# Kernel tuning notes

Hardware: AMD Instinct MI355X
Metric: run time of the kernel (lower is better)

The kernel has to match this reference:

```python
import jax, jax.numpy as jnp
import numpy as np

B = 4        # batch_size
S = 128      # input spatial grid size per dim (shape=[128,128,128])
C = 64       # feature channels
N = 500000   # active voxels
K = 2        # kernel_size == stride (non-overlapping sparse max pool)


def setup_inputs() -> dict:
    key = jax.random.key(0)
    kf, kb, ks = jax.random.split(key, 3)
    features = jax.random.normal(kf, (N, C), dtype=jnp.float32)
    b = jax.random.randint(kb, (N, 1), 0, B, dtype=jnp.int32)
    zyx = jax.random.randint(ks, (N, 3), 0, S, dtype=jnp.int32)
    coors = jnp.concatenate([b, zyx], axis=1)  # [N, 4] = (batch, z, y, x)
    return {"features": features, "coors": coors}


def reference(features, coors):
    # Layer 1: sparse 2x2x2/stride-2 max pool == segment-max over output voxel ids.
    S1 = S // K  # 64
    b = coors[:, 0]
    z = coors[:, 1] // K
    y = coors[:, 2] // K
    x = coors[:, 3] // K
    seg = ((b * S1 + z) * S1 + y) * S1 + x  # flat output-site id
    nseg = B * S1 * S1 * S1
    # scatter-max: empty segments become -inf (inactive sites)
    dense = jax.ops.segment_max(features, seg, num_segments=nseg)
    cnt = jax.ops.segment_sum(jnp.ones((N,), jnp.int32), seg, num_segments=nseg)
    mask1 = (cnt > 0).reshape(B, S1, S1, S1)
    dense = dense.reshape(B, S1, S1, S1, C)

    # Layer 2: same pooling on the (now grid-aligned) active sites.
    # -inf at inactive sites makes block-max equal to max over active sites only.
    S2 = S1 // K  # 32
    blocks = dense.reshape(B, S2, K, S2, K, S2, K, C)
    pooled = blocks.max(axis=(2, 4, 6))               # [B, S2, S2, S2, C]
    mask2 = mask1.reshape(B, S2, K, S2, K, S2, K).any(axis=(2, 4, 6))
    out = jnp.where(mask2[..., None], pooled, jnp.float32(0.0))
    return out
```

## Files before the change

kernel.cpp:

```cpp
#include <hip/hip_runtime.h>

#define NB 4
#define S_OUT 32
#define NC 64
#define OUT_CELLS (NB * S_OUT * S_OUT * S_OUT)
#define OUT_ELEMS (OUT_CELLS * NC)
#define NGROUPS (OUT_CELLS / 4)
#define CAP 16
#define OVF_CAP 65536

typedef float floatx4 __attribute__((ext_vector_type(4)));


__global__ void fill_kernel(const int4* __restrict__ coors,
                            int* __restrict__ cnt,
                            int* __restrict__ list,
                            int* __restrict__ ovf_cnt,
                            int* __restrict__ ovf,
                            int n_pts) {
    int p = blockIdx.x * blockDim.x + threadIdx.x;
    if (p >= n_pts) return;
    int4 co = coors[p];
    int cell = ((co.x * S_OUT + (co.y >> 2)) * S_OUT + (co.z >> 2)) * S_OUT + (co.w >> 2);
    int slot = atomicAdd(&cnt[cell], 1);
    if (slot < CAP) {
        list[cell * CAP + slot] = p;
    } else {
        int o = atomicAdd(ovf_cnt, 1);
        if (o < OVF_CAP) ovf[o] = p;
    }
}

__global__ __launch_bounds__(256) void gather_kernel(
        const float* __restrict__ features,
        const int4* __restrict__ coors,
        const int* __restrict__ cnt,
        const int* __restrict__ list,
        const int* __restrict__ ovf_cnt,
        const int* __restrict__ ovf,
        float* __restrict__ out) {
    const int lane  = threadIdx.x & 63;
    const int wid   = (blockIdx.x * blockDim.x + threadIdx.x) >> 6;
    const int nw    = (gridDim.x * blockDim.x) >> 6;
    const int cl    = (lane & 15) << 2;
    const int sbase = lane & 48;
    const int qsel  = lane >> 4;

    int g = wid;
    if (g >= NGROUPS) return;

    int n_pf  = cnt[(g << 2) + qsel];
    int pl_pf = list[((size_t)g << 6) + lane];

    while (true) {
        int n  = n_pf;
        int pl = pl_pf;
        int gn = g + nw;
        if (gn < NGROUPS) {
            n_pf  = cnt[(gn << 2) + qsel];
            pl_pf = list[((size_t)gn << 6) + lane];
        }

        int m = n < CAP ? n : CAP;
        float4 acc = make_float4(-INFINITY, -INFINITY, -INFINITY, -INFINITY);

        #pragma unroll
        for (int s = 0; s < 8; ++s) {
            int p = __shfl(pl, sbase + s);
            bool v = s < m;
            int ps = v ? p : 0;
            const float4 f = *(const float4*)(features + (size_t)ps * NC + cl);
            if (v) {
                acc.x = fmaxf(acc.x, f.x); acc.y = fmaxf(acc.y, f.y);
                acc.z = fmaxf(acc.z, f.z); acc.w = fmaxf(acc.w, f.w);
            }
        }
        if (m > 8) {
            for (int s = 8; s < m; ++s) {
                int p = __shfl(pl, sbase + s);
                const float4 f = *(const float4*)(features + (size_t)p * NC + cl);
                acc.x = fmaxf(acc.x, f.x); acc.y = fmaxf(acc.y, f.y);
                acc.z = fmaxf(acc.z, f.z); acc.w = fmaxf(acc.w, f.w);
            }
        }
        if (__builtin_expect(__any(n > CAP), 0)) {
            int mycell = (g << 2) + qsel;
            int novf = *ovf_cnt;
            if (novf > OVF_CAP) novf = OVF_CAP;
            for (int i = 0; i < novf; ++i) {
                int p = ovf[i];
                int4 co = coors[p];
                int cellp = ((co.x * S_OUT + (co.y >> 2)) * S_OUT + (co.z >> 2)) * S_OUT + (co.w >> 2);
                if (n > CAP && cellp == mycell) {
                    const float4 f = *(const float4*)(features + (size_t)p * NC + cl);
                    acc.x = fmaxf(acc.x, f.x); acc.y = fmaxf(acc.y, f.y);
                    acc.z = fmaxf(acc.z, f.z); acc.w = fmaxf(acc.w, f.w);
                }
            }
        }
        if (n == 0) acc = make_float4(0.f, 0.f, 0.f, 0.f);
        floatx4 accv = { acc.x, acc.y, acc.z, acc.w };
        __builtin_nontemporal_store(accv, (floatx4*)(out + ((size_t)g << 8) + (size_t)lane * 4));

        if (gn >= NGROUPS) break;
        g = gn;
    }
}


__device__ __forceinline__ unsigned flip_f(float f) {
    unsigned u = __float_as_uint(f);
    return (u & 0x80000000u) ? ~u : (u | 0x80000000u);
}
__device__ __forceinline__ float unflip_f(unsigned u) {
    unsigned v = (u & 0x80000000u) ? (u & 0x7FFFFFFFu) : ~u;
    return __uint_as_float(v);
}

__global__ void init_kernel(uint4* __restrict__ out4, int n4) {
    int i = blockIdx.x * blockDim.x + threadIdx.x;
    int stride = gridDim.x * blockDim.x;
    uint4 z = make_uint4(0u, 0u, 0u, 0u);
    for (; i < n4; i += stride) out4[i] = z;
}

__global__ void scatter_kernel(const float* __restrict__ features,
                               const int4* __restrict__ coors,
                               unsigned* __restrict__ acc, int n_pts) {
    int gid = blockIdx.x * blockDim.x + threadIdx.x;
    int p = gid >> 6;
    int c = threadIdx.x & 63;
    if (p >= n_pts) return;
    int4 co = coors[p];
    int cell = ((co.x * S_OUT + (co.y >> 2)) * S_OUT + (co.z >> 2)) * S_OUT + (co.w >> 2);
    atomicMax(acc + (size_t)cell * NC + c, flip_f(features[(size_t)p * NC + c]));
}

__global__ void finalize_kernel(unsigned* __restrict__ acc, int n) {
    int i = blockIdx.x * blockDim.x + threadIdx.x;
    int stride = gridDim.x * blockDim.x;
    for (; i < n; i += stride) {
        unsigned u = acc[i];
        ((float*)acc)[i] = (u == 0u) ? 0.0f : unflip_f(u);
    }
}

extern "C" void kernel_launch(void* const* d_in, const int* in_sizes, int n_in,
                              void* d_out, int out_size, void* d_ws, size_t ws_size,
                              hipStream_t stream) {
    const float* features = (const float*)d_in[0];
    const int4*  coors    = (const int4*)d_in[1];
    int n_pts = in_sizes[0] / NC;

    const size_t off_cnt  = 0;
    const size_t cnt_b    = (size_t)OUT_CELLS * 4;
    const size_t off_ovfc = cnt_b;
    const size_t off_ovf  = off_ovfc + 256;
    const size_t off_list = off_ovf + (size_t)OVF_CAP * 4;
    const size_t need     = off_list + (size_t)OUT_CELLS * CAP * 4;

    if (ws_size >= need) {
        char* ws = (char*)d_ws;
        int* cnt     = (int*)(ws + off_cnt);
        int* ovf_cnt = (int*)(ws + off_ovfc);
        int* ovf     = (int*)(ws + off_ovf);
        int* list    = (int*)(ws + off_list);
        float* out   = (float*)d_out;

        (void)hipMemsetAsync(ws, 0, off_ovfc + 4, stream);

        {
            int block = 256;
            int grid = (n_pts + block - 1) / block;
            fill_kernel<<<grid, block, 0, stream>>>(coors, cnt, list, ovf_cnt, ovf, n_pts);
        }
        {
            int block = 256;
            int grid = 2048;
            gather_kernel<<<grid, block, 0, stream>>>(features, coors, cnt, list,
                                                      ovf_cnt, ovf, out);
        }
    } else {
        unsigned* acc = (unsigned*)d_out;
        init_kernel<<<2048, 256, 0, stream>>>((uint4*)d_out, OUT_ELEMS / 4);
        int grid = (n_pts * 64 + 255) / 256;
        scatter_kernel<<<grid, 256, 0, stream>>>(features, coors, acc, n_pts);
        finalize_kernel<<<2048, 256, 0, stream>>>(acc, OUT_ELEMS);
    }
}
```

Before: 63.95 us.

## Software-pipeline gather kernel with double-buffered feature loads across four groups

Replaces the grid-stride loop in the gather kernel with a fully unrolled, fixed four-groups-per-wave schedule. Loads for the first eight points of the next group are issued into a second register set while the current group is reduced, so more memory requests stay in flight per wave. This assumes NGROUPS equals exactly four times the wave count, which holds for the hard-coded grid but drops the bounds check and raises register pressure, which may reduce occupancy.

```diff
diff --git a/kernel.cpp b/kernel.cpp
--- a/kernel.cpp
+++ b/kernel.cpp
@@ -8,6 +8,8 @@
 #define NGROUPS (OUT_CELLS / 4)
 #define CAP 16
 #define OVF_CAP 65536
+#define GATHER_BLOCKS 2048
+#define NWAVES (GATHER_BLOCKS * 4)
 
 typedef float floatx4 __attribute__((ext_vector_type(4)));
 
@@ -41,70 +43,88 @@
         float* __restrict__ out) {
     const int lane  = threadIdx.x & 63;
     const int wid   = (blockIdx.x * blockDim.x + threadIdx.x) >> 6;
-    const int nw    = (gridDim.x * blockDim.x) >> 6;
     const int cl    = (lane & 15) << 2;
     const int sbase = lane & 48;
     const int qsel  = lane >> 4;
 
-    int g = wid;
-    if (g >= NGROUPS) return;
-
-    int n_pf  = cnt[(g << 2) + qsel];
-    int pl_pf = list[((size_t)g << 6) + lane];
-
-    while (true) {
-        int n  = n_pf;
-        int pl = pl_pf;
-        int gn = g + nw;
-        if (gn < NGROUPS) {
-            n_pf  = cnt[(gn << 2) + qsel];
-            pl_pf = list[((size_t)gn << 6) + lane];
-        }
-
-        int m = n < CAP ? n : CAP;
-        float4 acc = make_float4(-INFINITY, -INFINITY, -INFINITY, -INFINITY);
-
-        #pragma unroll
-        for (int s = 0; s < 8; ++s) {
-            int p = __shfl(pl, sbase + s);
-            bool v = s < m;
-            int ps = v ? p : 0;
-            const float4 f = *(const float4*)(features + (size_t)ps * NC + cl);
-            if (v) {
-                acc.x = fmaxf(acc.x, f.x); acc.y = fmaxf(acc.y, f.y);
-                acc.z = fmaxf(acc.z, f.z); acc.w = fmaxf(acc.w, f.w);
-            }
-        }
-        if (m > 8) {
-            for (int s = 8; s < m; ++s) {
-                int p = __shfl(pl, sbase + s);
-                const float4 f = *(const float4*)(features + (size_t)p * NC + cl);
-                acc.x = fmaxf(acc.x, f.x); acc.y = fmaxf(acc.y, f.y);
-                acc.z = fmaxf(acc.z, f.z); acc.w = fmaxf(acc.w, f.w);
-            }
-        }
-        if (__builtin_expect(__any(n > CAP), 0)) {
-            int mycell = (g << 2) + qsel;
-            int novf = *ovf_cnt;
-            if (novf > OVF_CAP) novf = OVF_CAP;
-            for (int i = 0; i < novf; ++i) {
-                int p = ovf[i];
-                int4 co = coors[p];
-                int cellp = ((co.x * S_OUT + (co.y >> 2)) * S_OUT + (co.z >> 2)) * S_OUT + (co.w >> 2);
-                if (n > CAP && cellp == mycell) {
-                    const float4 f = *(const float4*)(features + (size_t)p * NC + cl);
-                    acc.x = fmaxf(acc.x, f.x); acc.y = fmaxf(acc.y, f.y);
-                    acc.z = fmaxf(acc.z, f.z); acc.w = fmaxf(acc.w, f.w);
-                }
-            }
-        }
-        if (n == 0) acc = make_float4(0.f, 0.f, 0.f, 0.f);
-        floatx4 accv = { acc.x, acc.y, acc.z, acc.w };
-        __builtin_nontemporal_store(accv, (floatx4*)(out + ((size_t)g << 8) + (size_t)lane * 4));
-
-        if (gn >= NGROUPS) break;
-        g = gn;
-    }
+#define META(i) \
+    const int g##i = wid + (i) * NWAVES; \
+    int n##i = cnt[(g##i << 2) + qsel]; \
+    int pl##i = list[((size_t)g##i << 6) + lane];
+    META(0) META(1) META(2) META(3)
+#undef META
+
+    float4 a0, a1, a2, a3, a4, a5, a6, a7;
+    float4 b0, b1, b2, b3, b4, b5, b6, b7;
+
+#define ISSUE(i, R0,R1,R2,R3,R4,R5,R6,R7) \
+    { \
+        int m_ = n##i < CAP ? n##i : CAP; \
+        int p_; \
+        p_ = __shfl(pl##i, sbase + 0); R0 = *(const float4*)(features + (size_t)(0 < m_ ? p_ : 0) * NC + cl); \
+        p_ = __shfl(pl##i, sbase + 1); R1 = *(const float4*)(features + (size_t)(1 < m_ ? p_ : 0) * NC + cl); \
+        p_ = __shfl(pl##i, sbase + 2); R2 = *(const float4*)(features + (size_t)(2 < m_ ? p_ : 0) * NC + cl); \
+        p_ = __shfl(pl##i, sbase + 3); R3 = *(const float4*)(features + (size_t)(3 < m_ ? p_ : 0) * NC + cl); \
+        p_ = __shfl(pl##i, sbase + 4); R4 = *(const float4*)(features + (size_t)(4 < m_ ? p_ : 0) * NC + cl); \
+        p_ = __shfl(pl##i, sbase + 5); R5 = *(const float4*)(features + (size_t)(5 < m_ ? p_ : 0) * NC + cl); \
+        p_ = __shfl(pl##i, sbase + 6); R6 = *(const float4*)(features + (size_t)(6 < m_ ? p_ : 0) * NC + cl); \
+        p_ = __shfl(pl##i, sbase + 7); R7 = *(const float4*)(features + (size_t)(7 < m_ ? p_ : 0) * NC + cl); \
+    }
+
+#define FM(ACC, F) \
+    ACC.x = fmaxf(ACC.x, F.x); ACC.y = fmaxf(ACC.y, F.y); \
+    ACC.z = fmaxf(ACC.z, F.z); ACC.w = fmaxf(ACC.w, F.w);
+
+#define CONSUME(i, R0,R1,R2,R3,R4,R5,R6,R7) \
+    { \
+        int m_ = n##i < CAP ? n##i : CAP; \
+        float4 acc = make_float4(-INFINITY, -INFINITY, -INFINITY, -INFINITY); \
+        if (0 < m_) { FM(acc, R0) } \
+        if (1 < m_) { FM(acc, R1) } \
+        if (2 < m_) { FM(acc, R2) } \
+        if (3 < m_) { FM(acc, R3) } \
+        if (4 < m_) { FM(acc, R4) } \
+        if (5 < m_) { FM(acc, R5) } \
+        if (6 < m_) { FM(acc, R6) } \
+        if (7 < m_) { FM(acc, R7) } \
+        if (__builtin_expect(m_ > 8, 0)) { \
+            for (int s_ = 8; s_ < m_; ++s_) { \
+                int p_ = __shfl(pl##i, sbase + s_); \
+                const float4 f_ = *(const float4*)(features + (size_t)p_ * NC + cl); \
+                FM(acc, f_) \
+            } \
+        } \
+        if (__builtin_expect(__any(n##i > CAP), 0)) { \
+            int mycell_ = (g##i << 2) + qsel; \
+            int novf_ = *ovf_cnt; \
+            if (novf_ > OVF_CAP) novf_ = OVF_CAP; \
+            for (int t_ = 0; t_ < novf_; ++t_) { \
+                int p_ = ovf[t_]; \
+                int4 co_ = coors[p_]; \
+                int cellp_ = ((co_.x * S_OUT + (co_.y >> 2)) * S_OUT + (co_.z >> 2)) * S_OUT + (co_.w >> 2); \
+                if (n##i > CAP && cellp_ == mycell_) { \
+                    const float4 f_ = *(const float4*)(features + (size_t)p_ * NC + cl); \
+                    FM(acc, f_) \
+                } \
+            } \
+        } \
+        if (n##i == 0) acc = make_float4(0.f, 0.f, 0.f, 0.f); \
+        floatx4 av_ = { acc.x, acc.y, acc.z, acc.w }; \
+        __builtin_nontemporal_store(av_, (floatx4*)(out + ((size_t)g##i << 8) + (size_t)lane * 4)); \
+    }
+
+    ISSUE(0, a0,a1,a2,a3,a4,a5,a6,a7)
+    ISSUE(1, b0,b1,b2,b3,b4,b5,b6,b7)
+    CONSUME(0, a0,a1,a2,a3,a4,a5,a6,a7)
+    ISSUE(2, a0,a1,a2,a3,a4,a5,a6,a7)
+    CONSUME(1, b0,b1,b2,b3,b4,b5,b6,b7)
+    ISSUE(3, b0,b1,b2,b3,b4,b5,b6,b7)
+    CONSUME(2, a0,a1,a2,a3,a4,a5,a6,a7)
+    CONSUME(3, b0,b1,b2,b3,b4,b5,b6,b7)
+
+#undef ISSUE
+#undef CONSUME
+#undef FM
 }
 
 
@@ -174,12 +194,8 @@
             int grid = (n_pts + block - 1) / block;
             fill_kernel<<<grid, block, 0, stream>>>(coors, cnt, list, ovf_cnt, ovf, n_pts);
         }
-        {
-            int block = 256;
-            int grid = 2048;
-            gather_kernel<<<grid, block, 0, stream>>>(features, coors, cnt, list,
-                                                      ovf_cnt, ovf, out);
-        }
+        gather_kernel<<<GATHER_BLOCKS, 256, 0, stream>>>(features, coors, cnt, list,
+                                                         ovf_cnt, ovf, out);
     } else {
         unsigned* acc = (unsigned*)d_out;
         init_kernel<<<2048, 256, 0, stream>>>((uint4*)d_out, OUT_ELEMS / 4);
```

Result: no change. 64.63 us (+1.1%).
